# Performance work log

Measured on AMD Instinct MI355X. Metric: run time of the kernel, lower is better.

Reference implementation:

```python
import jax, jax.numpy as jnp
import numpy as np
import math

G0, G1 = 24, 24           # initial/current grid size (command(initial_grid_size=(24,24), ...))
N = G0 * G1               # 576 spatial tokens
PREFIX = 1                # num_prefix_tokens (cls token)
EPS = 0.1                 # get_eps((24,24)): 0.5*23^2/0.1^2 = 26450 <= 32500, no doubling
COEF = float(max(G0, G1) ** 2)          # 576.0, sigmoid_fn coefficient
B_SHIFT = math.log(COEF - 1.0)          # b = log(575)
CLAMP = max(-0.5 * (max(G0, G1) - 1) ** 2, -6550.0)  # -264.5


def setup_inputs() -> dict:
    key = jax.random.key(0)
    k1, k2, k3 = jax.random.split(key, 3)
    head_dim = 64
    q = jax.random.normal(k1, (8, 12, N + PREFIX, head_dim), dtype=jnp.float32)
    W_var = jax.random.normal(k2, (head_dim, 2), dtype=jnp.float32) * (head_dim ** -0.5)
    b_var = jnp.zeros((2,), dtype=jnp.float32)
    W_alpha = jax.random.normal(k3, (head_dim, 1), dtype=jnp.float32) * (head_dim ** -0.5)
    b_alpha = jnp.zeros((1,), dtype=jnp.float32)
    return {"q": q, "W_var": W_var, "b_var": b_var, "W_alpha": W_alpha, "b_alpha": b_alpha}


def _gaussian_numerator():
    # coords: (N, 2) integer grid positions
    ii, jj = jnp.meshgrid(jnp.arange(G0), jnp.arange(G1), indexing="ij")
    coords = jnp.stack([ii, jj], axis=-1).reshape(N, 2).astype(jnp.float32)
    d = -0.5 * (coords[:, None, :] - coords[None, :, :]) ** 2  # (N, N, 2)
    return jnp.maximum(d, CLAMP)


def reference(q, W_var, b_var, W_alpha, b_alpha):
    qs = q[..., PREFIX:, :]                                   # (B, H, N, C)
    # var = coef * sigmoid(linear(q) - b), shape (B, H, N, 2)
    var = COEF * jax.nn.sigmoid(jnp.einsum("bhnc,ck->bhnk", qs, W_var) + b_var - B_SHIFT)
    # alpha = softplus(linear(q)), shape (B, H, N, 1)
    alpha = jax.nn.softplus(jnp.einsum("bhnc,ck->bhnk", qs, W_alpha) + b_alpha)
    d = _gaussian_numerator()                                 # (N, N, 2)
    # broadcast divide -> sum over coord dim -> exp: (B, H, N, N)
    gaussian = jnp.exp(jnp.sum(d[None, None] / (var[:, :, :, None, :] + EPS), axis=-1))
    addition = alpha * gaussian                               # alpha broadcasts over last dim
    # pad prefix rows/cols with 0 at the beginning -> (B, H, N+1, N+1)
    return jnp.pad(addition, ((0, 0), (0, 0), (PREFIX, 0), (PREFIX, 0)))
```

## Files before the change

### kernel.cpp

```cpp
#include <hip/hip_runtime.h>
#include <math.h>

#define G 24
#define NPTS (G * G)
#define ROWS (NPTS + 1)
#define HD 64
#define BH (8 * 12)
#define EPSF 0.1f
#define COEFF 576.0f
#define BSHIFT 6.3543700408f
#define RPB 8
#define BPI ((ROWS + RPB - 1) / RPB)

typedef float f32x4 __attribute__((ext_vector_type(4)));

__global__ __launch_bounds__(256) void gaussian_augment_kernel(
    const float* __restrict__ q,
    const float* __restrict__ Wv,
    const float* __restrict__ bv,
    const float* __restrict__ Wa,
    const float* __restrict__ ba,
    float* __restrict__ out)
{
    const int bh  = blockIdx.x / BPI;
    const int blk = blockIdx.x - bh * BPI;
    const int r0  = blk * RPB;
    const int Ract = min(RPB, ROWS - r0);
    const int tid = threadIdx.x;

    __shared__ float s_dot[RPB][3];
    __shared__ float s_par[RPB][3];
    __shared__ float s_ex0[RPB][G];
    __shared__ float s_ex1[RPB][G];
    __shared__ __align__(16) float s_row[RPB * ROWS + 4];

    const int wave = tid >> 6;
    const int lane = tid & 63;
    #pragma unroll
    for (int pass = 0; pass < 2; ++pass) {
        const int rr = wave + 4 * pass;
        if (rr < Ract) {
            const int r = r0 + rr;
            const float* qrow = q + ((size_t)bh * ROWS + r) * HD;
            const float qv = qrow[lane];
            float p0 = qv * Wv[2 * lane + 0];
            float p1 = qv * Wv[2 * lane + 1];
            float p2 = qv * Wa[lane];
            #pragma unroll
            for (int off = 32; off >= 1; off >>= 1) {
                p0 += __shfl_xor(p0, off);
                p1 += __shfl_xor(p1, off);
                p2 += __shfl_xor(p2, off);
            }
            if (lane == 0) {
                s_dot[rr][0] = p0;
                s_dot[rr][1] = p1;
                s_dot[rr][2] = p2;
            }
        }
    }
    __syncthreads();

    if (tid < Ract) {
        const int r = r0 + tid;
        const float x0 = s_dot[tid][0] + bv[0] - BSHIFT;
        const float x1 = s_dot[tid][1] + bv[1] - BSHIFT;
        const float xa = s_dot[tid][2] + ba[0];
        const float var0 = COEFF / (1.0f + expf(-x0));
        const float var1 = COEFF / (1.0f + expf(-x1));
        s_par[tid][0] = 1.0f / (var0 + EPSF);
        s_par[tid][1] = 1.0f / (var1 + EPSF);
        const float alpha = fmaxf(xa, 0.0f) + log1pf(expf(-fabsf(xa)));
        s_par[tid][2] = (r == 0) ? 0.0f : alpha;
    }
    __syncthreads();

    for (int e = tid; e < Ract * 48; e += 256) {
        const int rr = e / 48;
        const int k  = e - rr * 48;
        if (k < G) {
            const float t = (float)k;
            s_ex0[rr][k] = s_par[rr][2] * expf(-0.5f * t * t * s_par[rr][0]);
        } else {
            const float t = (float)(k - G);
            s_ex1[rr][k - G] = expf(-0.5f * t * t * s_par[rr][1]);
        }
    }
    __syncthreads();

    const size_t base = ((size_t)bh * ROWS + r0) * ROWS;
    const size_t S0   = base & ~(size_t)3;
    const int    off  = (int)(base - S0);

    for (int rr = 0; rr < Ract; ++rr) {
        const int r = r0 + rr;
        const int n = (r > 0) ? r - 1 : 0;
        const int in_ = n / G;
        const int jn_ = n - in_ * G;
        float* lrow = s_row + off + rr * ROWS;
        for (int c = tid; c < ROWS; c += 256) {
            float v = 0.0f;
            if (c > 0) {
                const int m  = c - 1;
                const int im = m / G;
                const int jm = m - im * G;
                const int di = (in_ > im) ? (in_ - im) : (im - in_);
                const int dj = (jn_ > jm) ? (jn_ - jm) : (jm - jn_);
                v = s_ex0[rr][di] * s_ex1[rr][dj];
            }
            lrow[c] = v;
        }
    }
    __syncthreads();

    const int span = Ract * ROWS;
    const size_t E = base + span;
    const int nch  = (int)((E - S0 + 3) >> 2);

    for (int idx = tid; idx < nch; idx += 256) {
        const size_t g0 = S0 + (size_t)4 * idx;
        if (g0 >= base && g0 + 4 <= E) {
            const f32x4 v = *(const f32x4*)&s_row[4 * idx];
            __builtin_nontemporal_store(v, (f32x4*)(out + g0));
        } else {
            #pragma unroll
            for (int t = 0; t < 4; ++t) {
                const size_t g = g0 + t;
                if (g >= base && g < E) out[g] = s_row[4 * idx + t];
            }
        }
    }
}

extern "C" void kernel_launch(void* const* d_in, const int* in_sizes, int n_in,
                              void* d_out, int out_size, void* d_ws, size_t ws_size,
                              hipStream_t stream) {
    const float* q  = (const float*)d_in[0];
    const float* Wv = (const float*)d_in[1];
    const float* bv = (const float*)d_in[2];
    const float* Wa = (const float*)d_in[3];
    const float* ba = (const float*)d_in[4];
    float* out = (float*)d_out;

    const int grid = BH * BPI;
    gaussian_augment_kernel<<<grid, 256, 0, stream>>>(q, Wv, bv, Wa, ba, out);
}
```

Baseline: 43.11 us.

## Write output rows directly from registers with per-row aligned vector stores

```diff
diff --git a/kernel.cpp b/kernel.cpp
--- a/kernel.cpp
+++ b/kernel.cpp
@@ -2,10 +2,9 @@
 #include <math.h>
 
 #define G 24
-#define NPTS (G * G)
-#define ROWS (NPTS + 1)
+#define ROWS 577
 #define HD 64
-#define BH (8 * 12)
+#define BH 96
 #define EPSF 0.1f
 #define COEFF 576.0f
 #define BSHIFT 6.3543700408f
@@ -30,9 +29,8 @@
 
     __shared__ float s_dot[RPB][3];
     __shared__ float s_par[RPB][3];
-    __shared__ float s_ex0[RPB][G];
-    __shared__ float s_ex1[RPB][G];
-    __shared__ __align__(16) float s_row[RPB * ROWS + 4];
+    __shared__ float s_ex0[RPB][32];
+    __shared__ float s_e1 [RPB][32];
 
     const int wave = tid >> 6;
     const int lane = tid & 63;
@@ -75,58 +73,87 @@
     }
     __syncthreads();
 
-    for (int e = tid; e < Ract * 48; e += 256) {
-        const int rr = e / 48;
-        const int k  = e - rr * 48;
-        if (k < G) {
-            const float t = (float)k;
-            s_ex0[rr][k] = s_par[rr][2] * expf(-0.5f * t * t * s_par[rr][0]);
-        } else {
-            const float t = (float)(k - G);
-            s_ex1[rr][k - G] = expf(-0.5f * t * t * s_par[rr][1]);
+    for (int e = tid; e < RPB * 64; e += 256) {
+        const int rr = e >> 6;
+        const int k  = e & 63;
+        if (rr < Ract) {
+            const int rg = r0 + rr;
+            const int n  = (rg > 0) ? rg - 1 : 0;
+            const int in_ = (int)((unsigned)n / 24u);
+            const int jn_ = n - in_ * 24;
+            if (k < 25) {
+                float v = 0.0f;
+                if (k < 24) {
+                    const float t = (float)(in_ - k);
+                    v = s_par[rr][2] * expf(-0.5f * t * t * s_par[rr][0]);
+                }
+                s_ex0[rr][k] = v;
+            } else if (k >= 32 && k < 60) {
+                const int j  = k - 32;
+                const int jm = (j >= 24) ? j - 24 : j;
+                const float t = (float)(jn_ - jm);
+                s_e1[rr][j] = expf(-0.5f * t * t * s_par[rr][1]);
+            }
         }
     }
     __syncthreads();
 
     const size_t base = ((size_t)bh * ROWS + r0) * ROWS;
-    const size_t S0   = base & ~(size_t)3;
-    const int    off  = (int)(base - S0);
 
-    for (int rr = 0; rr < Ract; ++rr) {
-        const int r = r0 + rr;
-        const int n = (r > 0) ? r - 1 : 0;
-        const int in_ = n / G;
-        const int jn_ = n - in_ * G;
-        float* lrow = s_row + off + rr * ROWS;
-        for (int c = tid; c < ROWS; c += 256) {
-            float v = 0.0f;
-            if (c > 0) {
-                const int m  = c - 1;
-                const int im = m / G;
-                const int jm = m - im * G;
-                const int di = (in_ > im) ? (in_ - im) : (im - in_);
-                const int dj = (jn_ > jm) ? (jn_ - jm) : (jm - jn_);
-                v = s_ex0[rr][di] * s_ex1[rr][dj];
+    if (tid < 8 * RPB) {
+        const int rr = tid >> 3;
+        const int s  = tid & 7;
+        if (rr < Ract) {
+            const size_t Sr = base + (size_t)rr * ROWS;
+            const int phi = (int)((4 - ((Sr + 1) & 3)) & 3);
+            const int F   = (576 - phi) >> 2;
+            if (s == 0) {
+                out[Sr] = 0.0f;
+            } else {
+                const int m = (s <= phi) ? (s - 1) : (4 * F + s - 1);
+                if (m < 576) {
+                    const int im = (int)((unsigned)m / 24u);
+                    const int jm = m - 24 * im;
+                    out[Sr + 1 + m] = s_ex0[rr][im] * s_e1[rr][jm];
+                }
             }
-            lrow[c] = v;
         }
     }
-    __syncthreads();
 
-    const int span = Ract * ROWS;
-    const size_t E = base + span;
-    const int nch  = (int)((E - S0 + 3) >> 2);
-
-    for (int idx = tid; idx < nch; idx += 256) {
-        const size_t g0 = S0 + (size_t)4 * idx;
-        if (g0 >= base && g0 + 4 <= E) {
-            const f32x4 v = *(const f32x4*)&s_row[4 * idx];
-            __builtin_nontemporal_store(v, (f32x4*)(out + g0));
-        } else {
+    {
+        const int rr = tid >> 5;
+        const int l  = tid & 31;
+        if (rr < Ract) {
+            const size_t Sr = base + (size_t)rr * ROWS;
+            const int phi = (int)((4 - ((Sr + 1) & 3)) & 3);
+            int m  = phi + 4 * l;
+            int im = (int)((unsigned)m / 24u);
+            int jm = m - 24 * im;
+            float* gp = out + Sr + 1 + m;
+            const float* e0p = s_ex0[rr];
+            const float* e1p = s_e1[rr];
             #pragma unroll
-            for (int t = 0; t < 4; ++t) {
-                const size_t g = g0 + t;
-                if (g >= base && g < E) out[g] = s_row[4 * idx + t];
+            for (int it = 0; it < 5; ++it) {
+                if (m <= 572) {
+                    const float x0  = e0p[im];
+                    const float x1  = e0p[im + 1];
+                    const float e1a = e1p[jm];
+                    const float e1b = e1p[jm + 1];
+                    const float e1c = e1p[jm + 2];
+                    const float e1d = e1p[jm + 3];
+                    f32x4 pk;
+                    pk[0] = x0 * e1a;
+                    pk[1] = (jm >= 23 ? x1 : x0) * e1b;
+                    pk[2] = (jm >= 22 ? x1 : x0) * e1c;
+                    pk[3] = (jm >= 21 ? x1 : x0) * e1d;
+                    __builtin_nontemporal_store(pk, (f32x4*)gp);
+                }
+                m  += 128;
+                jm += 8;
+                const bool w = (jm >= 24);
+                im += w ? 6 : 5;
+                jm -= w ? 24 : 0;
+                gp += 128;
             }
         }
     }
@@ -142,6 +169,5 @@
     const float* ba = (const float*)d_in[4];
     float* out = (float*)d_out;
 
-    const int grid = BH * BPI;
-    gaussian_augment_kernel<<<grid, 256, 0, stream>>>(q, Wv, bv, Wa, ba, out);
+    gaussian_augment_kernel<<<BH * BPI, 256, 0, stream>>>(q, Wv, bv, Wa, ba, out);
 }
```

New measurement: 37.74 us. 12.5% less time.
